# Performance work log

Hardware: AMD Instinct MI355X
Metric: run time of the kernel (lower is better)

Reference implementation:

```python
import jax, jax.numpy as jnp
import numpy as np

N, E, G = 20000, 320000, 1000
F_NODE, F_EDGE, HID, HEADS, NCLS = 12, 4, 64, 4, 4


def setup_inputs() -> dict:
    key = jax.random.key(0)
    ks = iter(jax.random.split(key, 64))

    def rn(shape, s=0.1):
        return jax.random.normal(next(ks), shape, jnp.float32) * s

    inp = {
        "x": rn((N, F_NODE), 1.0),
        "edge_index": jax.random.randint(next(ks), (2, E), 0, N, dtype=jnp.int32),
        "edge_attr": rn((E, F_EDGE), 1.0),
        "batch": jnp.sort(jax.random.randint(next(ks), (N,), 0, G, dtype=jnp.int32)),
    }
    # GATv2 layer params: lin_l (W,b), lin_r (W,b), lin_edge (W, no bias), att, out bias
    for i, (cin, H) in enumerate([(F_NODE, HEADS), (HID * HEADS, HEADS), (HID * HEADS, 1)], 1):
        d = H * HID
        inp[f"Wl{i}"] = rn((cin, d))
        inp[f"bl{i}"] = rn((d,))
        inp[f"Wr{i}"] = rn((cin, d))
        inp[f"br{i}"] = rn((d,))
        inp[f"We{i}"] = rn((F_EDGE, d))
        inp[f"att{i}"] = rn((H, HID))
        inp[f"bias{i}"] = rn((d,))
    inp["mW1"] = rn((HID, 32)); inp["mb1"] = rn((32,))
    inp["mW2"] = rn((32, 16)); inp["mb2"] = rn((16,))
    inp["mW3"] = rn((16, NCLS)); inp["mb3"] = rn((NCLS,))
    return inp


def gatv2(x, src, dst, ea, Wl, bl, Wr, br, We, att, bias, H):
    # PyG GATv2Conv (share_weights=False, negative_slope=0.2, concat=True, eval mode)
    xl = (x @ Wl + bl).reshape(N, H, HID)   # source transform
    xr = (x @ Wr + br).reshape(N, H, HID)   # target transform
    ee = (ea @ We).reshape(E, H, HID)       # edge embedding
    z = jax.nn.leaky_relu(xl[src] + xr[dst] + ee, 0.2)  # [E,H,C]
    logits = jnp.einsum("ehc,hc->eh", z, att)
    m = jax.ops.segment_max(logits, dst, num_segments=N)  # per-dest max
    ex = jnp.exp(logits - m[dst])
    denom = jax.ops.segment_sum(ex, dst, num_segments=N)
    alpha = ex / (denom[dst] + 1e-16)                      # segment softmax
    msg = (xl[src] * alpha[:, :, None]).reshape(E, H * HID)
    out = jax.ops.segment_sum(msg, dst, num_segments=N)
    return out + bias


def reference(x, edge_index, edge_attr, batch,
              Wl1, bl1, Wr1, br1, We1, att1, bias1,
              Wl2, bl2, Wr2, br2, We2, att2, bias2,
              Wl3, bl3, Wr3, br3, We3, att3, bias3,
              mW1, mb1, mW2, mb2, mW3, mb3):
    src, dst = edge_index[0], edge_index[1]
    h = jax.nn.elu(gatv2(x, src, dst, edge_attr, Wl1, bl1, Wr1, br1, We1, att1, bias1, HEADS))
    h = jax.nn.elu(gatv2(h, src, dst, edge_attr, Wl2, bl2, Wr2, br2, We2, att2, bias2, HEADS))
    h = gatv2(h, src, dst, edge_attr, Wl3, bl3, Wr3, br3, We3, att3, bias3, 1)  # [N,HID]
    # global mean pool
    sums = jax.ops.segment_sum(h, batch, num_segments=G)
    cnt = jax.ops.segment_sum(jnp.ones((N, 1), h.dtype), batch, num_segments=G)
    g = sums / jnp.maximum(cnt, 1.0)
    # MLP head (dropout disabled, eval mode)
    g = jax.nn.relu(g @ mW1 + mb1)
    g = jax.nn.relu(g @ mW2 + mb2)
    return g @ mW3 + mb3
```

## Files before the change

### kernel.cpp

```cpp
#include <hip/hip_runtime.h>
#include <hip/hip_bf16.h>

#define NNODES 20000
#define NEDGES 320000
#define NGRAPH 1000

typedef __hip_bfloat16 bf16;
typedef unsigned short u16;
typedef short short8 __attribute__((ext_vector_type(8)));
typedef float f32x4 __attribute__((ext_vector_type(4)));

__device__ __forceinline__ float b2f(bf16 x) { return __bfloat162float(x); }
__device__ __forceinline__ float bu2f(u16 u) { return __uint_as_float(((unsigned)u) << 16); }
__device__ __forceinline__ u16 f2bu(float v) {
    __hip_bfloat16 b = __float2bfloat16(v);
    return *reinterpret_cast<u16*>(&b);
}

__device__ __forceinline__ int rfl(int v) { return __builtin_amdgcn_readfirstlane(v); }

__device__ __forceinline__ float rowsum16(float v) {
    v += __int_as_float(__builtin_amdgcn_update_dpp(0, __float_as_int(v), 0x128, 0xF, 0xF, true));
    v += __int_as_float(__builtin_amdgcn_update_dpp(0, __float_as_int(v), 0x124, 0xF, 0xF, true));
    v += __int_as_float(__builtin_amdgcn_update_dpp(0, __float_as_int(v), 0x122, 0xF, 0xF, true));
    v += __int_as_float(__builtin_amdgcn_update_dpp(0, __float_as_int(v), 0x121, 0xF, 0xF, true));
    return v;
}

__device__ __forceinline__ int idx_at(const void* p, int i, int is64) {
    return is64 ? (int)((const long long*)p)[i] : ((const int*)p)[i];
}

__device__ __forceinline__ float raw_at(const void* p, size_t i, bool isbf) {
    return isbf ? b2f(((const bf16*)p)[i]) : ((const float*)p)[i];
}

static inline char* align16(char* p) {
    return (char*)(((uintptr_t)p + 15) & ~(uintptr_t)15);
}

__global__ void sniff_all(const void* __restrict__ x, const void* __restrict__ ei,
                          const void* __restrict__ batch, int* __restrict__ flags) {
    __shared__ int sb[4];
    if (threadIdx.x < 4) sb[threadIdx.x] = 0;
    __syncthreads();
    int gb = 0, gf = 0, ze = 0, zb = 0;
    for (int i = threadIdx.x; i < 8192; i += blockDim.x) {
        float vb = b2f(((const bf16*)x)[i]);
        float vf = ((const float*)x)[i];
        if (fabsf(vb) < 1e4f) gb++;
        if (fabsf(vf) < 1e4f) gf++;
        if (((const int*)ei)[2 * i + 1] == 0) ze++;
        if (((const int*)batch)[2 * i + 1] == 0) zb++;
    }
    atomicAdd(&sb[0], gb); atomicAdd(&sb[1], gf);
    atomicAdd(&sb[2], ze); atomicAdd(&sb[3], zb);
    __syncthreads();
    if (threadIdx.x == 0) {
        flags[0] = (sb[0] >= sb[1]) ? 1 : 0;
        flags[1] = (sb[2] > 6000) ? 1 : 0;
        flags[2] = (sb[3] > 6000) ? 1 : 0;
    }
}

struct Segs {
    const void* src[29];
    int off[30];
};

__device__ __forceinline__ void wtp_store(u16* __restrict__ dst, const void* __restrict__ src,
                                          int K, int N, int i, bool isbf) {
    int j = i & 7;
    int lane = (i >> 3) & 63;
    int rest = i >> 9;
    int KB = K >> 5;
    int tile = rest / KB, kbi = rest - tile * KB;
    int l16 = lane & 15, quad = lane >> 4;
    int n = tile * 16 + l16;
    int kk = kbi * 32 + quad * 8 + j;
    dst[i] = f2bu(raw_at(src, (size_t)kk * N + n, isbf));
}

__global__ void preprocess(Segs S, const int* __restrict__ flags,
                           float* __restrict__ conv, int total,
                           u16* __restrict__ eah,
                           u16* __restrict__ wt2l, u16* __restrict__ wt2r,
                           u16* __restrict__ wt3l, u16* __restrict__ wt3r,
                           int* __restrict__ deg, float* __restrict__ poolcnt) {
    int i = blockIdx.x * blockDim.x + threadIdx.x;
    bool isbf = flags[0] != 0;
    if (i < total) {
        int lo = 0, hi = 29;
        while (hi - lo > 1) {
            int mid = (lo + hi) >> 1;
            if (i >= S.off[mid]) lo = mid; else hi = mid;
        }
        conv[i] = raw_at(S.src[lo], i - S.off[lo], isbf);
        return;
    }
    i -= total;
    if (i < NEDGES * 4) {
        eah[i] = isbf ? ((const u16*)S.src[1])[i] : f2bu(((const float*)S.src[1])[i]);
        return;
    }
    i -= NEDGES * 4;
    if (i < 65536) { wtp_store(wt2l, S.src[9],  256, 256, i, isbf); return; }
    i -= 65536;
    if (i < 65536) { wtp_store(wt2r, S.src[11], 256, 256, i, isbf); return; }
    i -= 65536;
    if (i < 16384) { wtp_store(wt3l, S.src[16], 256, 64, i, isbf); return; }
    i -= 16384;
    if (i < 16384) { wtp_store(wt3r, S.src[18], 256, 64, i, isbf); return; }
    i -= 16384;
    if (i < NNODES) { deg[i] = 0; return; }
    i -= NNODES;
    if (i < NGRAPH * 65) poolcnt[i] = 0.f;
}

__global__ void csr_hist(const void* __restrict__ ei, const int* __restrict__ flags,
                         int* __restrict__ deg) {
    int e = blockIdx.x * blockDim.x + threadIdx.x;
    if (e >= NEDGES) return;
    atomicAdd(&deg[idx_at(ei, NEDGES + e, flags[1])], 1);
}

__global__ void csr_scan(const int* __restrict__ deg, int* __restrict__ rowptr,
                         int* __restrict__ cursor) {
    __shared__ int wsum[16];
    __shared__ int wpre[16];
    const int t = threadIdx.x;
    const int wid = t >> 6, lane = t & 63;
    const int base = t * 20;
    int loc[20];
    int s = 0;
#pragma unroll
    for (int j = 0; j < 20; j++) {
        int i = base + j;
        int v = (i < NNODES) ? deg[i] : 0;
        loc[j] = s;
        s += v;
    }
    int incl = s;
#pragma unroll
    for (int o = 1; o < 64; o <<= 1) {
        int n = __shfl_up(incl, o);
        if (lane >= o) incl += n;
    }
    if (lane == 63) wsum[wid] = incl;
    __syncthreads();
    if (wid == 0 && lane < 16) {
        int v = wsum[lane];
        int inc2 = v;
#pragma unroll
        for (int o = 1; o < 16; o <<= 1) {
            int n = __shfl_up(inc2, o);
            if (lane >= o) inc2 += n;
        }
        wpre[lane] = inc2 - v;
    }
    __syncthreads();
    int excl = wpre[wid] + incl - s;
#pragma unroll
    for (int j = 0; j < 20; j++) {
        int i = base + j;
        if (i < NNODES) { rowptr[i] = excl + loc[j]; cursor[i] = excl + loc[j]; }
    }
    if (t == 1023) rowptr[NNODES] = excl + s;
}

__global__ void csr_scatter(const void* __restrict__ ei, const int* __restrict__ flags,
                            int* __restrict__ cursor, int2* __restrict__ csr) {
    int e = blockIdx.x * blockDim.x + threadIdx.x;
    if (e >= NEDGES) return;
    const int i64 = flags[1];
    int src = idx_at(ei, e, i64), dst = idx_at(ei, NEDGES + e, i64);
    int pos = atomicAdd(&cursor[dst], 1);
    csr[pos] = make_int2(src, e);
}

template <int TM, int CIN, int DOUT, bool GUARD>
__global__ __launch_bounds__(256, 2) void lin_gemm(
        const float* __restrict__ X,
        const float* __restrict__ Wl, const float* __restrict__ bl,
        const float* __restrict__ Wr, const float* __restrict__ br,
        u16* __restrict__ XL, float* __restrict__ XR) {
    constexpr int CPT = DOUT / 4;
    constexpr int RG = 256 / CPT;
    constexpr int M = RG * TM;
    __shared__ float xs[M * CIN];

    const int t = threadIdx.x;
    const int ct = t % CPT;
    const int rg = t / CPT;
    const int c0 = ct * 4;
    const int r0 = blockIdx.x * M;

    constexpr int C4 = CIN / 4;
    for (int i = t; i < M * C4; i += 256) {
        int r = i / C4, j = i - r * C4;
        float4 v = make_float4(0.f, 0.f, 0.f, 0.f);
        if (!GUARD || (r0 + r) < NNODES)
            v = *(const float4*)&X[(size_t)(r0 + r) * CIN + j * 4];
        *(float4*)&xs[r * CIN + j * 4] = v;
    }
    __syncthreads();

    float4 accL[TM], accR[TM];
#pragma unroll
    for (int m = 0; m < TM; m++) {
        accL[m] = make_float4(0.f, 0.f, 0.f, 0.f);
        accR[m] = make_float4(0.f, 0.f, 0.f, 0.f);
    }
    const float* xbase = &xs[rg * TM * CIN];
#pragma unroll 4
    for (int k = 0; k < CIN; k++) {
        const float4 wl = *(const float4*)&Wl[k * DOUT + c0];
        const float4 wr = *(const float4*)&Wr[k * DOUT + c0];
#pragma unroll
        for (int m = 0; m < TM; m++) {
            float xv = xbase[m * CIN + k];
            accL[m].x = fmaf(xv, wl.x, accL[m].x);
            accL[m].y = fmaf(xv, wl.y, accL[m].y);
            accL[m].z = fmaf(xv, wl.z, accL[m].z);
            accL[m].w = fmaf(xv, wl.w, accL[m].w);
            accR[m].x = fmaf(xv, wr.x, accR[m].x);
            accR[m].y = fmaf(xv, wr.y, accR[m].y);
            accR[m].z = fmaf(xv, wr.z, accR[m].z);
            accR[m].w = fmaf(xv, wr.w, accR[m].w);
        }
    }

    const float4 b4l = *(const float4*)&bl[c0];
    const float4 b4r = *(const float4*)&br[c0];
#pragma unroll
    for (int m = 0; m < TM; m++) {
        int row = r0 + rg * TM + m;
        if (GUARD && row >= NNODES) continue;
        float l0 = accL[m].x + b4l.x, l1 = accL[m].y + b4l.y;
        float l2 = accL[m].z + b4l.z, l3 = accL[m].w + b4l.w;
        uint2 pk;
        pk.x = (unsigned)f2bu(l0) | ((unsigned)f2bu(l1) << 16);
        pk.y = (unsigned)f2bu(l2) | ((unsigned)f2bu(l3) << 16);
        *(uint2*)&XL[(size_t)row * DOUT + c0] = pk;
        float4 r4;
        r4.x = accR[m].x + b4r.x; r4.y = accR[m].y + b4r.y;
        r4.z = accR[m].z + b4r.z; r4.w = accR[m].w + b4r.w;
        *(float4*)&XR[(size_t)row * DOUT + c0] = r4;
    }
}

template <int N>
__global__ __launch_bounds__(256) void lin_gemm_mfma(
        const float* __restrict__ X,
        const u16* __restrict__ WlP, const float* __restrict__ bl,
        const u16* __restrict__ WrP, const float* __restrict__ br,
        u16* __restrict__ XL, float* __restrict__ XR) {
    constexpr int K = 256;
    constexpr int KB = K / 32;
    constexpr int NTW = N / 64;
    constexpr int XSTR = 264;
    __shared__ u16 xhi[16 * XSTR];
    __shared__ u16 xlo[16 * XSTR];

    const int t = threadIdx.x;
    const int w = t >> 6, lane = t & 63;
    const int quad = lane >> 4, l16 = lane & 15;
    const int m0 = blockIdx.x * 16;
    const int nbase = w * (N / 4);

    for (int idx = t; idx < 16 * 64; idx += 256) {
        int r = idx >> 6, c4 = idx & 63;
        float4 v = *(const float4*)&X[(size_t)(m0 + r) * K + c4 * 4];
        float f[4] = {v.x, v.y, v.z, v.w};
        ushort4 hi, lo;
        u16 h;
        h = f2bu(f[0]); hi.x = h; lo.x = f2bu(f[0] - bu2f(h));
        h = f2bu(f[1]); hi.y = h; lo.y = f2bu(f[1] - bu2f(h));
        h = f2bu(f[2]); hi.z = h; lo.z = f2bu(f[2] - bu2f(h));
        h = f2bu(f[3]); hi.w = h; lo.w = f2bu(f[3] - bu2f(h));
        *(ushort4*)&xhi[r * XSTR + c4 * 4] = hi;
        *(ushort4*)&xlo[r * XSTR + c4 * 4] = lo;
    }
    __syncthreads();

    f32x4 accL[NTW], accR[NTW];
#pragma unroll
    for (int i = 0; i < NTW; i++) {
        accL[i] = (f32x4){0.f, 0.f, 0.f, 0.f};
        accR[i] = (f32x4){0.f, 0.f, 0.f, 0.f};
    }

    const int abase = l16 * XSTR + quad * 8;
#pragma unroll
    for (int kbi = 0; kbi < KB; kbi++) {
        short8 ahi = *(const short8*)&xhi[abase + kbi * 32];
        short8 alo = *(const short8*)&xlo[abase + kbi * 32];
#pragma unroll
        for (int i = 0; i < NTW; i++) {
            int tg = (nbase >> 4) + i;
            size_t off = ((size_t)(tg * KB + kbi) * 64 + lane) * 8;
            short8 bL = *(const short8*)&WlP[off];
            short8 bR = *(const short8*)&WrP[off];
            accL[i] = __builtin_amdgcn_mfma_f32_16x16x32_bf16(ahi, bL, accL[i], 0, 0, 0);
            accL[i] = __builtin_amdgcn_mfma_f32_16x16x32_bf16(alo, bL, accL[i], 0, 0, 0);
            accR[i] = __builtin_amdgcn_mfma_f32_16x16x32_bf16(ahi, bR, accR[i], 0, 0, 0);
            accR[i] = __builtin_amdgcn_mfma_f32_16x16x32_bf16(alo, bR, accR[i], 0, 0, 0);
        }
    }

#pragma unroll
    for (int i = 0; i < NTW; i++) {
        int col = nbase + i * 16 + l16;
        float bLv = bl[col], bRv = br[col];
#pragma unroll
        for (int r = 0; r < 4; r++) {
            int row = m0 + quad * 4 + r;
            XL[(size_t)row * N + col] = f2bu(accL[i][r] + bLv);
            XR[(size_t)row * N + col] = accR[i][r] + bRv;
        }
    }
}

template <bool ELU>
__global__ __launch_bounds__(256, 2) void gat_agg_mw(
        const int* __restrict__ rowptr, const int2* __restrict__ csr,
        const u16* __restrict__ XL, const float* __restrict__ XR,
        const u16* __restrict__ eah,
        const float* __restrict__ We, const float* __restrict__ att,
        const float* __restrict__ bias, float* __restrict__ out) {
    const int lane = threadIdx.x & 63;
    const int dst = rfl(blockIdx.x * 4 + (threadIdx.x >> 6));
    const int c0 = lane * 4;

    const float4 w0 = *(const float4*)&We[0 * 256 + c0];
    const float4 w1 = *(const float4*)&We[1 * 256 + c0];
    const float4 w2 = *(const float4*)&We[2 * 256 + c0];
    const float4 w3 = *(const float4*)&We[3 * 256 + c0];
    const float4 at = *(const float4*)&att[c0];
    const float4 xr = *(const float4*)&XR[(size_t)dst * 256 + c0];
    const uint2* __restrict__ eah2 = (const uint2*)eah;

    const int i0 = rfl(rowptr[dst]);
    const int i1 = rfl(rowptr[dst + 1]);

    float l = 0.f;
    float4 acc = make_float4(0.f, 0.f, 0.f, 0.f);

#define MW_BODY(XU, A0, A1, A2, A3)                                              \
    {                                                                            \
        float xl0 = __uint_as_float((XU).x << 16);                               \
        float xl1 = __uint_as_float((XU).x & 0xffff0000u);                       \
        float xl2 = __uint_as_float((XU).y << 16);                               \
        float xl3 = __uint_as_float((XU).y & 0xffff0000u);                       \
        float z0 = fmaf(A0, w0.x, fmaf(A1, w1.x, fmaf(A2, w2.x, fmaf(A3, w3.x, xl0 + xr.x)))); \
        float z1 = fmaf(A0, w0.y, fmaf(A1, w1.y, fmaf(A2, w2.y, fmaf(A3, w3.y, xl1 + xr.y)))); \
        float z2 = fmaf(A0, w0.z, fmaf(A1, w1.z, fmaf(A2, w2.z, fmaf(A3, w3.z, xl2 + xr.z)))); \
        float z3 = fmaf(A0, w0.w, fmaf(A1, w1.w, fmaf(A2, w2.w, fmaf(A3, w3.w, xl3 + xr.w)))); \
        z0 = fmaxf(z0, 0.2f * z0);                                               \
        z1 = fmaxf(z1, 0.2f * z1);                                               \
        z2 = fmaxf(z2, 0.2f * z2);                                               \
        z3 = fmaxf(z3, 0.2f * z3);                                               \
        float v = fmaf(z3, at.w, fmaf(z2, at.z, fmaf(z1, at.y, z0 * at.x)));     \
        v = rowsum16(v);                                                         \
        float p = __expf(v);                                                     \
        l += p;                                                                  \
        acc.x = fmaf(p, xl0, acc.x);                                             \
        acc.y = fmaf(p, xl1, acc.y);                                             \
        acc.z = fmaf(p, xl2, acc.z);                                             \
        acc.w = fmaf(p, xl3, acc.w);                                             \
    }

    int e = i0;
    for (; e + 4 <= i1; e += 4) {
        int2 t0 = csr[e + 0];
        int2 t1 = csr[e + 1];
        int2 t2 = csr[e + 2];
        int2 t3 = csr[e + 3];
        int sx0 = rfl(t0.x), sy0 = rfl(t0.y);
        int sx1 = rfl(t1.x), sy1 = rfl(t1.y);
        int sx2 = rfl(t2.x), sy2 = rfl(t2.y);
        int sx3 = rfl(t3.x), sy3 = rfl(t3.y);
        uint2 xu0 = *(const uint2*)&XL[(size_t)sx0 * 256 + c0];
        uint2 xu1 = *(const uint2*)&XL[(size_t)sx1 * 256 + c0];
        uint2 xu2 = *(const uint2*)&XL[(size_t)sx2 * 256 + c0];
        uint2 xu3 = *(const uint2*)&XL[(size_t)sx3 * 256 + c0];
        uint2 au0 = eah2[sy0];
        uint2 au1 = eah2[sy1];
        uint2 au2 = eah2[sy2];
        uint2 au3 = eah2[sy3];
        float a00 = __uint_as_float(rfl(au0.x << 16));
        float a01 = __uint_as_float(rfl(au0.x & 0xffff0000u));
        float a02 = __uint_as_float(rfl(au0.y << 16));
        float a03 = __uint_as_float(rfl(au0.y & 0xffff0000u));
        float a10 = __uint_as_float(rfl(au1.x << 16));
        float a11 = __uint_as_float(rfl(au1.x & 0xffff0000u));
        float a12 = __uint_as_float(rfl(au1.y << 16));
        float a13 = __uint_as_float(rfl(au1.y & 0xffff0000u));
        float a20 = __uint_as_float(rfl(au2.x << 16));
        float a21 = __uint_as_float(rfl(au2.x & 0xffff0000u));
        float a22 = __uint_as_float(rfl(au2.y << 16));
        float a23 = __uint_as_float(rfl(au2.y & 0xffff0000u));
        float a30 = __uint_as_float(rfl(au3.x << 16));
        float a31 = __uint_as_float(rfl(au3.x & 0xffff0000u));
        float a32 = __uint_as_float(rfl(au3.y << 16));
        float a33 = __uint_as_float(rfl(au3.y & 0xffff0000u));
        MW_BODY(xu0, a00, a01, a02, a03)
        MW_BODY(xu1, a10, a11, a12, a13)
        MW_BODY(xu2, a20, a21, a22, a23)
        MW_BODY(xu3, a30, a31, a32, a33)
    }
    for (; e < i1; ++e) {
        int2 t = csr[e];
        int sx = rfl(t.x), sy = rfl(t.y);
        uint2 xu = *(const uint2*)&XL[(size_t)sx * 256 + c0];
        uint2 au = eah2[sy];
        float a0 = __uint_as_float(rfl(au.x << 16));
        float a1 = __uint_as_float(rfl(au.x & 0xffff0000u));
        float a2 = __uint_as_float(rfl(au.y << 16));
        float a3 = __uint_as_float(rfl(au.y & 0xffff0000u));
        MW_BODY(xu, a0, a1, a2, a3)
    }
#undef MW_BODY

    float inv = 1.f / (l + 1e-16f);
    const float4 b4 = *(const float4*)&bias[c0];
    float o0 = fmaf(acc.x, inv, b4.x);
    float o1 = fmaf(acc.y, inv, b4.y);
    float o2 = fmaf(acc.z, inv, b4.z);
    float o3 = fmaf(acc.w, inv, b4.w);
    if (ELU) {
        o0 = o0 > 0.f ? o0 : expf(o0) - 1.f;
        o1 = o1 > 0.f ? o1 : expf(o1) - 1.f;
        o2 = o2 > 0.f ? o2 : expf(o2) - 1.f;
        o3 = o3 > 0.f ? o3 : expf(o3) - 1.f;
    }
    *(float4*)&out[(size_t)dst * 256 + c0] = make_float4(o0, o1, o2, o3);
}

template <int H, bool ELU, bool POOLF>
__global__ __launch_bounds__(H * 64, 4) void gat_agg(
                        const int* __restrict__ rowptr, const int2* __restrict__ csr,
                        const u16* __restrict__ XL, const float* __restrict__ XR,
                        const u16* __restrict__ eah,
                        const float* __restrict__ We, const float* __restrict__ att,
                        const float* __restrict__ bias, float* __restrict__ out,
                        const void* __restrict__ batch, const int* __restrict__ flags,
                        float* __restrict__ pool, float* __restrict__ cnt) {
    const int Dout = H * 64;
    const int dst = blockIdx.x;
    const int t = threadIdx.x;
    const int h = t >> 6;
    const int lane = t & 63;
    const int g = lane >> 4;
    const int k = lane & 15;
    const int c0 = h * 64 + k * 4;

    const float4 w0 = *(const float4*)&We[0 * Dout + c0];
    const float4 w1 = *(const float4*)&We[1 * Dout + c0];
    const float4 w2 = *(const float4*)&We[2 * Dout + c0];
    const float4 w3 = *(const float4*)&We[3 * Dout + c0];
    const float4 at = *(const float4*)&att[c0];
    const float4 xr = *(const float4*)&XR[dst * Dout + c0];

    const int i0 = rowptr[dst], i1 = rowptr[dst + 1];
    const int niter = (i1 - i0 + 3) >> 2;

    float l = 0.f;
    float4 acc = make_float4(0.f, 0.f, 0.f, 0.f);

#define GAT_EDGE_BODY(E_IDX)                                                     \
    {                                                                            \
        int e_ = (E_IDX);                                                        \
        bool valid_ = e_ < i1;                                                   \
        int2 se_ = csr[valid_ ? e_ : i0];                                        \
        uint2 xu_ = *(const uint2*)&XL[se_.x * Dout + c0];                       \
        uint2 au_ = *(const uint2*)&eah[se_.y * 4];                              \
        float xl0_ = __uint_as_float(xu_.x << 16);                               \
        float xl1_ = __uint_as_float(xu_.x & 0xffff0000u);                       \
        float xl2_ = __uint_as_float(xu_.y << 16);                               \
        float xl3_ = __uint_as_float(xu_.y & 0xffff0000u);                       \
        float A0_ = __uint_as_float(au_.x << 16);                                \
        float A1_ = __uint_as_float(au_.x & 0xffff0000u);                        \
        float A2_ = __uint_as_float(au_.y << 16);                                \
        float A3_ = __uint_as_float(au_.y & 0xffff0000u);                        \
        float z0_ = fmaf(A0_, w0.x, fmaf(A1_, w1.x, fmaf(A2_, w2.x, fmaf(A3_, w3.x, xl0_ + xr.x)))); \
        float z1_ = fmaf(A0_, w0.y, fmaf(A1_, w1.y, fmaf(A2_, w2.y, fmaf(A3_, w3.y, xl1_ + xr.y)))); \
        float z2_ = fmaf(A0_, w0.z, fmaf(A1_, w1.z, fmaf(A2_, w2.z, fmaf(A3_, w3.z, xl2_ + xr.z)))); \
        float z3_ = fmaf(A0_, w0.w, fmaf(A1_, w1.w, fmaf(A2_, w2.w, fmaf(A3_, w3.w, xl3_ + xr.w)))); \
        z0_ = fmaxf(z0_, 0.2f * z0_);                                            \
        z1_ = fmaxf(z1_, 0.2f * z1_);                                            \
        z2_ = fmaxf(z2_, 0.2f * z2_);                                            \
        z3_ = fmaxf(z3_, 0.2f * z3_);                                            \
        float v_ = fmaf(z3_, at.w, fmaf(z2_, at.z, fmaf(z1_, at.y, z0_ * at.x))); \
        v_ += __shfl_xor(v_, 1);                                                 \
        v_ += __shfl_xor(v_, 2);                                                 \
        v_ += __shfl_xor(v_, 4);                                                 \
        v_ += __shfl_xor(v_, 8);                                                 \
        float p_ = valid_ ? __expf(v_) : 0.f;                                    \
        l += p_;                                                                 \
        acc.x = fmaf(p_, xl0_, acc.x);                                           \
        acc.y = fmaf(p_, xl1_, acc.y);                                           \
        acc.z = fmaf(p_, xl2_, acc.z);                                           \
        acc.w = fmaf(p_, xl3_, acc.w);                                           \
    }

    int it = 0;
    for (; it + 2 <= niter; it += 2) {
        int eb = i0 + g + it * 4;
        GAT_EDGE_BODY(eb)
        GAT_EDGE_BODY(eb + 4)
    }
    if (it < niter) {
        GAT_EDGE_BODY(i0 + g + it * 4)
    }
#undef GAT_EDGE_BODY

    l += __shfl_xor(l, 16);      l += __shfl_xor(l, 32);
    acc.x += __shfl_xor(acc.x, 16); acc.x += __shfl_xor(acc.x, 32);
    acc.y += __shfl_xor(acc.y, 16); acc.y += __shfl_xor(acc.y, 32);
    acc.z += __shfl_xor(acc.z, 16); acc.z += __shfl_xor(acc.z, 32);
    acc.w += __shfl_xor(acc.w, 16); acc.w += __shfl_xor(acc.w, 32);

    if (g == 0) {
        float inv = 1.f / (l + 1e-16f);
        const float4 b4 = *(const float4*)&bias[c0];
        float o0 = fmaf(acc.x, inv, b4.x);
        float o1 = fmaf(acc.y, inv, b4.y);
        float o2 = fmaf(acc.z, inv, b4.z);
        float o3 = fmaf(acc.w, inv, b4.w);
        if (ELU) {
            o0 = o0 > 0.f ? o0 : expf(o0) - 1.f;
            o1 = o1 > 0.f ? o1 : expf(o1) - 1.f;
            o2 = o2 > 0.f ? o2 : expf(o2) - 1.f;
            o3 = o3 > 0.f ? o3 : expf(o3) - 1.f;
        }
        if (POOLF) {
            int b = idx_at(batch, dst, flags[2]);
            atomicAdd(&pool[b * 64 + c0 + 0], o0);
            atomicAdd(&pool[b * 64 + c0 + 1], o1);
            atomicAdd(&pool[b * 64 + c0 + 2], o2);
            atomicAdd(&pool[b * 64 + c0 + 3], o3);
            if (lane == 0) atomicAdd(&cnt[b], 1.f);
        } else {
            *(float4*)&out[dst * Dout + c0] = make_float4(o0, o1, o2, o3);
        }
    }
}

__global__ void mlp_head(const float* __restrict__ pool, const float* __restrict__ cnt,
                         const float* __restrict__ mW1, const float* __restrict__ mb1,
                         const float* __restrict__ mW2, const float* __restrict__ mb2,
                         const float* __restrict__ mW3, const float* __restrict__ mb3,
                         float* __restrict__ out) {
    __shared__ float g[64], s1[32], s2[16];
    int b = blockIdx.x, t = threadIdx.x;
    float c = fmaxf(cnt[b], 1.f);
    g[t] = pool[b * 64 + t] / c;
    __syncthreads();
    if (t < 32) {
        float a = 0.f;
        for (int k = 0; k < 64; k++) a = fmaf(g[k], mW1[k * 32 + t], a);
        s1[t] = fmaxf(a + mb1[t], 0.f);
    }
    __syncthreads();
    if (t < 16) {
        float a = 0.f;
        for (int k = 0; k < 32; k++) a = fmaf(s1[k], mW2[k * 16 + t], a);
        s2[t] = fmaxf(a + mb2[t], 0.f);
    }
    __syncthreads();
    if (t < 4) {
        float a = 0.f;
        for (int k = 0; k < 16; k++) a = fmaf(s2[k], mW3[k * 4 + t], a);
        out[b * 4 + t] = a + mb3[t];
    }
}


extern "C" void kernel_launch(void* const* d_in, const int* in_sizes, int n_in,
                              void* d_out, int out_size, void* d_ws, size_t ws_size,
                              hipStream_t stream) {
    const void* ei    = d_in[1];
    const void* batch = d_in[3];

    int fidx[29];
    fidx[0] = 0;
    fidx[1] = 2;
    for (int i = 0; i < 21; i++) fidx[2 + i] = 4 + i;
    for (int i = 0; i < 6; i++) fidx[23 + i] = 25 + i;

    Segs S;
    int off = 0;
    for (int i = 0; i < 29; i++) {
        S.src[i] = d_in[fidx[i]];
        S.off[i] = off;
        off += in_sizes[fidx[i]];
    }
    S.off[29] = off;
    const int total = off;

    char* p = (char*)d_ws;
    int*   FLAGS  = (int*)p;                 p += 16;
    float* CONV   = (float*)p;               p += sizeof(float) * total;  p = align16(p);
    int*   DEG    = (int*)p;                 p += sizeof(int) * NNODES;
    int*   ROWPTR = (int*)p;                 p += sizeof(int) * (NNODES + 1);
    int*   CURSOR = (int*)p;                 p += sizeof(int) * (NNODES + 1);  p = align16(p);
    int2*  CSR    = (int2*)p;                p += sizeof(int2) * NEDGES;  p = align16(p);
    u16*   EAH    = (u16*)p;                 p += sizeof(u16) * NEDGES * 4;  p = align16(p);
    u16*   WT2L   = (u16*)p;                 p += sizeof(u16) * 256 * 256;
    u16*   WT2R   = (u16*)p;                 p += sizeof(u16) * 256 * 256;
    u16*   WT3L   = (u16*)p;                 p += sizeof(u16) * 64 * 256;
    u16*   WT3R   = (u16*)p;                 p += sizeof(u16) * 64 * 256;  p = align16(p);
    u16*   XLb    = (u16*)p;                 p += sizeof(u16) * NNODES * 256;  p = align16(p);
    float* XRb    = (float*)p;               p += sizeof(float) * NNODES * 256;
    float* ACC    = (float*)p;               p += sizeof(float) * NNODES * 256;
    float* POOL   = (float*)p;               p += sizeof(float) * NGRAPH * 64;
    float* CNT    = (float*)p;               p += sizeof(float) * NGRAPH;

    const float* CX  = CONV + S.off[0];
    const float* CP[21];
    for (int i = 0; i < 21; i++) CP[i] = CONV + S.off[2 + i];
    const float* CmW1 = CONV + S.off[23];
    const float* Cmb1 = CONV + S.off[24];
    const float* CmW2 = CONV + S.off[25];
    const float* Cmb2 = CONV + S.off[26];
    const float* CmW3 = CONV + S.off[27];
    const float* Cmb3 = CONV + S.off[28];

    sniff_all<<<1, 256, 0, stream>>>(d_in[0], ei, batch, FLAGS);
    int pre_total = total + NEDGES * 4 + 65536 * 2 + 16384 * 2 + NNODES + NGRAPH * 65;
    preprocess<<<(pre_total + 255) / 256, 256, 0, stream>>>(
        S, FLAGS, CONV, total, EAH, WT2L, WT2R, WT3L, WT3R, DEG, POOL);

    csr_hist<<<(NEDGES + 255) / 256, 256, 0, stream>>>(ei, FLAGS, DEG);
    csr_scan<<<1, 1024, 0, stream>>>(DEG, ROWPTR, CURSOR);
    csr_scatter<<<(NEDGES + 255) / 256, 256, 0, stream>>>(ei, FLAGS, CURSOR, CSR);

    lin_gemm<4, 12, 256, false><<<NNODES / 16, 256, 0, stream>>>(CX, CP[0], CP[1], CP[2], CP[3], XLb, XRb);
    gat_agg_mw<true><<<NNODES / 4, 256, 0, stream>>>(ROWPTR, CSR, XLb, XRb, EAH,
        CP[4], CP[5], CP[6], ACC);

    lin_gemm_mfma<256><<<NNODES / 16, 256, 0, stream>>>(ACC, WT2L, CP[8], WT2R, CP[10], XLb, XRb);
    gat_agg_mw<true><<<NNODES / 4, 256, 0, stream>>>(ROWPTR, CSR, XLb, XRb, EAH,
        CP[11], CP[12], CP[13], ACC);

    lin_gemm_mfma<64><<<NNODES / 16, 256, 0, stream>>>(ACC, WT3L, CP[15], WT3R, CP[17], XLb, XRb);
    gat_agg<1, false, true><<<NNODES, 64, 0, stream>>>(ROWPTR, CSR, XLb, XRb, EAH,
        CP[18], CP[19], CP[20], ACC, batch, FLAGS, POOL, CNT);

    mlp_head<<<NGRAPH, 64, 0, stream>>>(POOL, CNT, CmW1, Cmb1, CmW2, Cmb2, CmW3, Cmb3, (float*)d_out);
}
```

Baseline: 368.5 us.

## Remap layer-3 aggregation to one destination per 16-lane group

Replaces the single-head aggregation kernel, which ran one 64-thread block per destination with four lanes-groups splitting edges, with a kernel in which each 16-lane group owns a whole destination and walks its edges serially. Sixteen destinations share a 256-thread block. This removes the cross-group shuffle reductions and uses DPP row sums for the attention dot product. It also cuts the number of tiny blocks. In exchange, groups in a wave iterate to the max degree of their four destinations, which wastes lanes when degrees differ, and the pool atomics are now issued by every lane.

```diff
diff --git a/kernel.cpp b/kernel.cpp
--- a/kernel.cpp
+++ b/kernel.cpp
@@ -437,114 +437,105 @@
     *(float4*)&out[(size_t)dst * 256 + c0] = make_float4(o0, o1, o2, o3);
 }
 
-template <int H, bool ELU, bool POOLF>
-__global__ __launch_bounds__(H * 64, 4) void gat_agg(
-                        const int* __restrict__ rowptr, const int2* __restrict__ csr,
-                        const u16* __restrict__ XL, const float* __restrict__ XR,
-                        const u16* __restrict__ eah,
-                        const float* __restrict__ We, const float* __restrict__ att,
-                        const float* __restrict__ bias, float* __restrict__ out,
-                        const void* __restrict__ batch, const int* __restrict__ flags,
-                        float* __restrict__ pool, float* __restrict__ cnt) {
-    const int Dout = H * 64;
-    const int dst = blockIdx.x;
+__global__ __launch_bounds__(256, 4) void gat_agg_mw1(
+        const int* __restrict__ rowptr, const int2* __restrict__ csr,
+        const u16* __restrict__ XL, const float* __restrict__ XR,
+        const u16* __restrict__ eah,
+        const float* __restrict__ We, const float* __restrict__ att,
+        const float* __restrict__ bias,
+        const void* __restrict__ batch, const int* __restrict__ flags,
+        float* __restrict__ pool, float* __restrict__ cnt) {
     const int t = threadIdx.x;
-    const int h = t >> 6;
+    const int w = t >> 6;
     const int lane = t & 63;
     const int g = lane >> 4;
     const int k = lane & 15;
-    const int c0 = h * 64 + k * 4;
-
-    const float4 w0 = *(const float4*)&We[0 * Dout + c0];
-    const float4 w1 = *(const float4*)&We[1 * Dout + c0];
-    const float4 w2 = *(const float4*)&We[2 * Dout + c0];
-    const float4 w3 = *(const float4*)&We[3 * Dout + c0];
+    const int c0 = k * 4;
+    const int dst = blockIdx.x * 16 + w * 4 + g;
+
+    const float4 w0 = *(const float4*)&We[0 * 64 + c0];
+    const float4 w1 = *(const float4*)&We[1 * 64 + c0];
+    const float4 w2 = *(const float4*)&We[2 * 64 + c0];
+    const float4 w3 = *(const float4*)&We[3 * 64 + c0];
     const float4 at = *(const float4*)&att[c0];
-    const float4 xr = *(const float4*)&XR[dst * Dout + c0];
-
-    const int i0 = rowptr[dst], i1 = rowptr[dst + 1];
-    const int niter = (i1 - i0 + 3) >> 2;
+    const float4 xr = *(const float4*)&XR[(size_t)dst * 64 + c0];
+    const uint2* __restrict__ eah2 = (const uint2*)eah;
+
+    const int i0 = rowptr[dst];
+    const int i1 = rowptr[dst + 1];
+    const int niter = i1 - i0;
+    int mx = niter;
+    mx = max(mx, __shfl_xor(mx, 16));
+    mx = max(mx, __shfl_xor(mx, 32));
 
     float l = 0.f;
     float4 acc = make_float4(0.f, 0.f, 0.f, 0.f);
 
-#define GAT_EDGE_BODY(E_IDX)                                                     \
+#define MW1_BODY(VALID, XU, AU)                                                  \
     {                                                                            \
-        int e_ = (E_IDX);                                                        \
-        bool valid_ = e_ < i1;                                                   \
-        int2 se_ = csr[valid_ ? e_ : i0];                                        \
-        uint2 xu_ = *(const uint2*)&XL[se_.x * Dout + c0];                       \
-        uint2 au_ = *(const uint2*)&eah[se_.y * 4];                              \
-        float xl0_ = __uint_as_float(xu_.x << 16);                               \
-        float xl1_ = __uint_as_float(xu_.x & 0xffff0000u);                       \
-        float xl2_ = __uint_as_float(xu_.y << 16);                               \
-        float xl3_ = __uint_as_float(xu_.y & 0xffff0000u);                       \
-        float A0_ = __uint_as_float(au_.x << 16);                                \
-        float A1_ = __uint_as_float(au_.x & 0xffff0000u);                        \
-        float A2_ = __uint_as_float(au_.y << 16);                                \
-        float A3_ = __uint_as_float(au_.y & 0xffff0000u);                        \
-        float z0_ = fmaf(A0_, w0.x, fmaf(A1_, w1.x, fmaf(A2_, w2.x, fmaf(A3_, w3.x, xl0_ + xr.x)))); \
-        float z1_ = fmaf(A0_, w0.y, fmaf(A1_, w1.y, fmaf(A2_, w2.y, fmaf(A3_, w3.y, xl1_ + xr.y)))); \
-        float z2_ = fmaf(A0_, w0.z, fmaf(A1_, w1.z, fmaf(A2_, w2.z, fmaf(A3_, w3.z, xl2_ + xr.z)))); \
-        float z3_ = fmaf(A0_, w0.w, fmaf(A1_, w1.w, fmaf(A2_, w2.w, fmaf(A3_, w3.w, xl3_ + xr.w)))); \
-        z0_ = fmaxf(z0_, 0.2f * z0_);                                            \
-        z1_ = fmaxf(z1_, 0.2f * z1_);                                            \
-        z2_ = fmaxf(z2_, 0.2f * z2_);                                            \
-        z3_ = fmaxf(z3_, 0.2f * z3_);                                            \
-        float v_ = fmaf(z3_, at.w, fmaf(z2_, at.z, fmaf(z1_, at.y, z0_ * at.x))); \
-        v_ += __shfl_xor(v_, 1);                                                 \
-        v_ += __shfl_xor(v_, 2);                                                 \
-        v_ += __shfl_xor(v_, 4);                                                 \
-        v_ += __shfl_xor(v_, 8);                                                 \
-        float p_ = valid_ ? __expf(v_) : 0.f;                                    \
-        l += p_;                                                                 \
-        acc.x = fmaf(p_, xl0_, acc.x);                                           \
-        acc.y = fmaf(p_, xl1_, acc.y);                                           \
-        acc.z = fmaf(p_, xl2_, acc.z);                                           \
-        acc.w = fmaf(p_, xl3_, acc.w);                                           \
-    }
-
+        float xl0 = __uint_as_float((XU).x << 16);                               \
+        float xl1 = __uint_as_float((XU).x & 0xffff0000u);                       \
+        float xl2 = __uint_as_float((XU).y << 16);                               \
+        float xl3 = __uint_as_float((XU).y & 0xffff0000u);                       \
+        float A0 = __uint_as_float((AU).x << 16);                                \
+        float A1 = __uint_as_float((AU).x & 0xffff0000u);                        \
+        float A2 = __uint_as_float((AU).y << 16);                                \
+        float A3 = __uint_as_float((AU).y & 0xffff0000u);                        \
+        float z0 = fmaf(A0, w0.x, fmaf(A1, w1.x, fmaf(A2, w2.x, fmaf(A3, w3.x, xl0 + xr.x)))); \
+        float z1 = fmaf(A0, w0.y, fmaf(A1, w1.y, fmaf(A2, w2.y, fmaf(A3, w3.y, xl1 + xr.y)))); \
+        float z2 = fmaf(A0, w0.z, fmaf(A1, w1.z, fmaf(A2, w2.z, fmaf(A3, w3.z, xl2 + xr.z)))); \
+        float z3 = fmaf(A0, w0.w, fmaf(A1, w1.w, fmaf(A2, w2.w, fmaf(A3, w3.w, xl3 + xr.w)))); \
+        z0 = fmaxf(z0, 0.2f * z0);                                               \
+        z1 = fmaxf(z1, 0.2f * z1);                                               \
+        z2 = fmaxf(z2, 0.2f * z2);                                               \
+        z3 = fmaxf(z3, 0.2f * z3);                                               \
+        float v = fmaf(z3, at.w, fmaf(z2, at.z, fmaf(z1, at.y, z0 * at.x)));     \
+        v = rowsum16(v);                                                         \
+        float p = (VALID) ? __expf(v) : 0.f;                                     \
+        l += p;                                                                  \
+        acc.x = fmaf(p, xl0, acc.x);                                             \
+        acc.y = fmaf(p, xl1, acc.y);                                             \
+        acc.z = fmaf(p, xl2, acc.z);                                             \
+        acc.w = fmaf(p, xl3, acc.w);                                             \
+    }
+
+    const int esafe = min(i0, NEDGES - 1);
     int it = 0;
-    for (; it + 2 <= niter; it += 2) {
-        int eb = i0 + g + it * 4;
-        GAT_EDGE_BODY(eb)
-        GAT_EDGE_BODY(eb + 4)
-    }
-    if (it < niter) {
-        GAT_EDGE_BODY(i0 + g + it * 4)
-    }
-#undef GAT_EDGE_BODY
-
-    l += __shfl_xor(l, 16);      l += __shfl_xor(l, 32);
-    acc.x += __shfl_xor(acc.x, 16); acc.x += __shfl_xor(acc.x, 32);
-    acc.y += __shfl_xor(acc.y, 16); acc.y += __shfl_xor(acc.y, 32);
-    acc.z += __shfl_xor(acc.z, 16); acc.z += __shfl_xor(acc.z, 32);
-    acc.w += __shfl_xor(acc.w, 16); acc.w += __shfl_xor(acc.w, 32);
-
-    if (g == 0) {
-        float inv = 1.f / (l + 1e-16f);
-        const float4 b4 = *(const float4*)&bias[c0];
-        float o0 = fmaf(acc.x, inv, b4.x);
-        float o1 = fmaf(acc.y, inv, b4.y);
-        float o2 = fmaf(acc.z, inv, b4.z);
-        float o3 = fmaf(acc.w, inv, b4.w);
-        if (ELU) {
-            o0 = o0 > 0.f ? o0 : expf(o0) - 1.f;
-            o1 = o1 > 0.f ? o1 : expf(o1) - 1.f;
-            o2 = o2 > 0.f ? o2 : expf(o2) - 1.f;
-            o3 = o3 > 0.f ? o3 : expf(o3) - 1.f;
-        }
-        if (POOLF) {
-            int b = idx_at(batch, dst, flags[2]);
-            atomicAdd(&pool[b * 64 + c0 + 0], o0);
-            atomicAdd(&pool[b * 64 + c0 + 1], o1);
-            atomicAdd(&pool[b * 64 + c0 + 2], o2);
-            atomicAdd(&pool[b * 64 + c0 + 3], o3);
-            if (lane == 0) atomicAdd(&cnt[b], 1.f);
-        } else {
-            *(float4*)&out[dst * Dout + c0] = make_float4(o0, o1, o2, o3);
-        }
-    }
+    for (; it + 2 <= mx; it += 2) {
+        int ea = i0 + it, eb = i0 + it + 1;
+        bool va = ea < i1, vb = eb < i1;
+        int2 sa = csr[va ? ea : esafe];
+        int2 sb = csr[vb ? eb : esafe];
+        uint2 xua = *(const uint2*)&XL[(size_t)sa.x * 64 + c0];
+        uint2 xub = *(const uint2*)&XL[(size_t)sb.x * 64 + c0];
+        uint2 aua = eah2[sa.y];
+        uint2 aub = eah2[sb.y];
+        MW1_BODY(va, xua, aua)
+        MW1_BODY(vb, xub, aub)
+    }
+    if (it < mx) {
+        int ea = i0 + it;
+        bool va = ea < i1;
+        int2 sa = csr[va ? ea : esafe];
+        uint2 xua = *(const uint2*)&XL[(size_t)sa.x * 64 + c0];
+        uint2 aua = eah2[sa.y];
+        MW1_BODY(va, xua, aua)
+    }
+#undef MW1_BODY
+
+    float inv = 1.f / (l + 1e-16f);
+    const float4 b4 = *(const float4*)&bias[c0];
+    float o0 = fmaf(acc.x, inv, b4.x);
+    float o1 = fmaf(acc.y, inv, b4.y);
+    float o2 = fmaf(acc.z, inv, b4.z);
+    float o3 = fmaf(acc.w, inv, b4.w);
+
+    int b = idx_at(batch, dst, flags[2]);
+    atomicAdd(&pool[b * 64 + c0 + 0], o0);
+    atomicAdd(&pool[b * 64 + c0 + 1], o1);
+    atomicAdd(&pool[b * 64 + c0 + 2], o2);
+    atomicAdd(&pool[b * 64 + c0 + 3], o3);
+    if (k == 0) atomicAdd(&cnt[b], 1.f);
 }
 
 __global__ void mlp_head(const float* __restrict__ pool, const float* __restrict__ cnt,
@@ -645,8 +636,8 @@
         CP[11], CP[12], CP[13], ACC);
 
     lin_gemm_mfma<64><<<NNODES / 16, 256, 0, stream>>>(ACC, WT3L, CP[15], WT3R, CP[17], XLb, XRb);
-    gat_agg<1, false, true><<<NNODES, 64, 0, stream>>>(ROWPTR, CSR, XLb, XRb, EAH,
-        CP[18], CP[19], CP[20], ACC, batch, FLAGS, POOL, CNT);
+    gat_agg_mw1<<<NNODES / 16, 256, 0, stream>>>(ROWPTR, CSR, XLb, XRb, EAH,
+        CP[18], CP[19], CP[20], batch, FLAGS, POOL, CNT);
 
     mlp_head<<<NGRAPH, 64, 0, stream>>>(POOL, CNT, CmW1, Cmb1, CmW2, Cmb2, CmW3, Cmb3, (float*)d_out);
 }
```

Result: slower. 377.3 us (+2.4%).
